# Kernel optimization log

Hardware: AMD Instinct MI355X
Metric: run time of the kernel (lower is better)

The kernel has to match this reference:

```python
import jax, jax.numpy as jnp
import numpy as np

HEADS = 16
DIM_HEAD = 64
SCALE = DIM_HEAD ** -0.5


def setup_inputs() -> dict:
    key = jax.random.key(0)
    k1, k2, k3 = jax.random.split(key, 3)
    dim = 1024
    inner = HEADS * DIM_HEAD  # 1024
    x = jax.random.normal(k1, (4, 2048, dim), dtype=jnp.float32)
    # Dense kernels stored as [in, out] like keras; scaled for sane magnitudes
    w_qkv = jax.random.normal(k2, (dim, inner * 3), dtype=jnp.float32) * (dim ** -0.5)
    w_out = jax.random.normal(k3, (inner, dim), dtype=jnp.float32) * (inner ** -0.5)
    b_out = jnp.zeros((dim,), dtype=jnp.float32)
    return {"x": x, "w_qkv": w_qkv, "w_out": w_out, "b_out": b_out}


def reference(x, w_qkv, w_out, b_out):
    b, n, _ = x.shape
    qkv = x @ w_qkv  # [b, n, 3*inner]
    q, k, v = jnp.split(qkv, 3, axis=-1)
    # 'b n (h d) -> b h n d'
    split_heads = lambda t: t.reshape(b, n, HEADS, DIM_HEAD).transpose(0, 2, 1, 3)
    q, k, v = split_heads(q), split_heads(k), split_heads(v)
    dots = jnp.einsum('bhid,bhjd->bhij', q, k) * SCALE  # [b,h,n,n]
    attn = jax.nn.softmax(dots, axis=-1)
    out = jnp.einsum('bhij,bhjd->bhid', attn, v)  # [b,h,n,d]
    out = out.transpose(0, 2, 1, 3).reshape(b, n, HEADS * DIM_HEAD)  # 'b h n d -> b n (h d)'
    # project_out: Dense(dim) + Dropout(0.0) (no-op)
    return out @ w_out + b_out
```

## Files before the change

kernel.cpp:

```cpp
#include <hip/hip_runtime.h>
#include <hip/hip_bf16.h>
#include <stdint.h>

#define BATCH 4
#define SEQ   2048
#define HEADS 16
#define DHEAD 64
#define DIM   1024
#define NQKV  3072
#define ROWS  (BATCH*SEQ)
#define QSCALE 0.18033688011112042f
#define SMAX 12.0f

typedef __attribute__((ext_vector_type(8)))  short short8;
typedef __attribute__((ext_vector_type(4)))  float f32x4;
typedef __attribute__((ext_vector_type(16))) float f32x16;

#if __has_builtin(__builtin_amdgcn_exp2f)
#define EXP2F(x) __builtin_amdgcn_exp2f(x)
#else
#define EXP2F(x) __expf((x) * 0.6931471805599453f)
#endif

typedef const __attribute__((address_space(1))) uint32_t GU32;
typedef __attribute__((address_space(3))) uint32_t LU32;
#define GLLDS16(g, l) __builtin_amdgcn_global_load_lds((GU32*)(g), (LU32*)(l), 16, 0, 0)

__device__ __forceinline__ ushort f2bf(float f) {
    union { float f; uint32_t u; } x; x.f = f;
    uint32_t r = x.u + 0x7fffu + ((x.u >> 16) & 1u);
    return (ushort)(r >> 16);
}

__global__ __launch_bounds__(256) void cvt_x_kernel(
    const float* __restrict__ in, ushort* __restrict__ out, int n8) {
    int i = blockIdx.x * 256 + threadIdx.x;
    if (i >= n8) return;
    f32x4 a = ((const f32x4*)in)[2*i];
    f32x4 b = ((const f32x4*)in)[2*i+1];
    short8 o;
    o[0]=(short)f2bf(a[0]); o[1]=(short)f2bf(a[1]); o[2]=(short)f2bf(a[2]); o[3]=(short)f2bf(a[3]);
    o[4]=(short)f2bf(b[0]); o[5]=(short)f2bf(b[1]); o[6]=(short)f2bf(b[2]); o[7]=(short)f2bf(b[3]);
    ((short8*)out)[i] = o;
}

__global__ __launch_bounds__(256) void transpose_w_kernel(
    const float* __restrict__ in, ushort* __restrict__ out, int R, int C) {
    __shared__ float tile[32][33];
    int ctiles = C >> 5;
    int bx = blockIdx.x % ctiles, by = blockIdx.x / ctiles;
    int c0 = bx << 5, r0 = by << 5;
    int tx = threadIdx.x & 31, ty = threadIdx.x >> 5;
#pragma unroll
    for (int it = 0; it < 4; ++it)
        tile[ty + 8*it][tx] = in[(size_t)(r0 + ty + 8*it)*C + c0 + tx];
    __syncthreads();
#pragma unroll
    for (int it = 0; it < 4; ++it)
        out[(size_t)(c0 + ty + 8*it)*R + r0 + tx] = f2bf(tile[tx][ty + 8*it]);
}

__global__ __launch_bounds__(256) void gemm1_kernel(
    const ushort* __restrict__ A, const ushort* __restrict__ BT,
    ushort* __restrict__ Qo, ushort* __restrict__ Ko, ushort* __restrict__ Vt) {
    const int K = DIM;
    __shared__ ushort As[128][32];
    __shared__ ushort Bs[128][32];
    int t = threadIdx.x;
    int lane = t & 63, wid = t >> 6;
    int lo = lane & 15, hi = lane >> 4;
    int wm = wid >> 1, wn = wid & 1;
    int bx = blockIdx.x % (NQKV/128), by = blockIdx.x / (NQKV/128);
    int m0 = by * 128, n0 = bx * 128;
    int sr = t >> 2, sc = (t & 3) * 8;

    const ushort* ga = A  + (size_t)(m0 + sr) * K + sc;
    const ushort* gb = BT + (size_t)(n0 + sr) * K + sc;
    char* asb = (char*)&As[0][0] + wid * 1024;
    char* bsb = (char*)&Bs[0][0] + wid * 1024;

    f32x4 acc[4][4];
#pragma unroll
    for (int i = 0; i < 4; ++i)
#pragma unroll
        for (int j = 0; j < 4; ++j) acc[i][j] = (f32x4){0.f,0.f,0.f,0.f};

    for (int k0 = 0; k0 < K; k0 += 32) {
        __syncthreads();
        GLLDS16(ga + k0,                asb);
        GLLDS16(ga + (size_t)64*K + k0, asb + 4096);
        GLLDS16(gb + k0,                bsb);
        GLLDS16(gb + (size_t)64*K + k0, bsb + 4096);
        __syncthreads();
        short8 af[4], bf[4];
#pragma unroll
        for (int i = 0; i < 4; ++i) af[i] = *(const short8*)&As[wm*64 + i*16 + lo][hi*8];
#pragma unroll
        for (int j = 0; j < 4; ++j) bf[j] = *(const short8*)&Bs[wn*64 + j*16 + lo][hi*8];
#pragma unroll
        for (int i = 0; i < 4; ++i)
#pragma unroll
            for (int j = 0; j < 4; ++j)
                acc[i][j] = __builtin_amdgcn_mfma_f32_16x16x32_bf16(af[i], bf[j], acc[i][j], 0, 0, 0);
    }

#pragma unroll
    for (int i = 0; i < 4; ++i) {
#pragma unroll
        for (int j = 0; j < 4; ++j) {
            int col = n0 + wn*64 + j*16 + lo;
            int which = col >> 10, cc = col & 1023;
            int h_ = cc >> 6, d_ = cc & 63;
            int rb = m0 + wm*64 + i*16 + hi*4;
            int b_ = rb >> 11, n_ = rb & 2047;
            if (which == 2) {
                uint2 w;
                w.x = (uint32_t)f2bf(acc[i][j][0]) | ((uint32_t)f2bf(acc[i][j][1]) << 16);
                w.y = (uint32_t)f2bf(acc[i][j][2]) | ((uint32_t)f2bf(acc[i][j][3]) << 16);
                *(uint2*)&Vt[(((size_t)(b_*HEADS + h_))*DHEAD + d_)*SEQ + n_] = w;
            } else {
                ushort* dst = (which == 0) ? Qo : Ko;
                float scl = (which == 0) ? QSCALE : 1.0f;
#pragma unroll
                for (int r = 0; r < 4; ++r)
                    dst[(((size_t)(b_*HEADS + h_))*SEQ + n_ + r)*DHEAD + d_] = f2bf(acc[i][j][r] * scl);
            }
        }
    }
}

__global__ __launch_bounds__(256, 2) void attn_kernel(
    const ushort* __restrict__ Q, const ushort* __restrict__ K,
    const ushort* __restrict__ VT, ushort* __restrict__ O) {
    __shared__ ushort Ks[2][8192];

    int t = threadIdx.x;
    int lane = t & 63, wid = t >> 6;
    int l31 = lane & 31, l5 = lane >> 5;
    int bid = blockIdx.x;
    int bh = bid & 63, qb = bid >> 6;
    int q0 = qb * 256 + wid * 64;

    const ushort* QbA = Q  + (size_t)bh * SEQ * DHEAD + (size_t)(q0 + l31) * DHEAD + l5*8;
    const ushort* QbB = QbA + (size_t)32 * DHEAD;
    const ushort* Kbh = K  + (size_t)bh * SEQ * DHEAD;
    const ushort* V0  = VT + (size_t)bh * DHEAD * SEQ + (size_t)l31 * SEQ + l5*8;
    const ushort* V1  = V0 + (size_t)32 * SEQ;

    int rr = t >> 3, c8 = t & 7;
    short8 kreg[4];
#define GLOADK(TT) do { _Pragma("unroll") \
    for (int i = 0; i < 4; ++i) \
        kreg[i] = *(const short8*)(Kbh + ((size_t)((TT)*128 + i*32 + rr))*64 + c8*8); \
} while(0)
#define SWRITEK(BUF) do { _Pragma("unroll") \
    for (int i = 0; i < 4; ++i) \
        *(short8*)((char*)&Ks[BUF][0] + (i*32 + rr)*128 + ((c8*16) ^ ((rr&7)<<4))) = kreg[i]; \
} while(0)

    short8 qfA[4], qfB[4];
#pragma unroll
    for (int ds = 0; ds < 4; ++ds) {
        qfA[ds] = *(const short8*)(QbA + ds*16);
        qfB[ds] = *(const short8*)(QbB + ds*16);
    }

    f32x16 oaA0, oaA1, oaB0, oaB1;
#pragma unroll
    for (int r = 0; r < 16; ++r) { oaA0[r]=0.f; oaA1[r]=0.f; oaB0[r]=0.f; oaB1[r]=0.f; }
    float lA = 0.f, lB = 0.f;

    auto softmax_repack = [&](f32x16& st, float& l_, short8& P1o, short8& P2o) {
        float p[16];
#pragma unroll
        for (int r = 0; r < 16; ++r) p[r] = EXP2F(st[r] - SMAX);
        float s0 = (p[0]+p[1]) + (p[2]+p[3]);
        float s1 = (p[4]+p[5]) + (p[6]+p[7]);
        float s2 = (p[8]+p[9]) + (p[10]+p[11]);
        float s3 = (p[12]+p[13]) + (p[14]+p[15]);
        l_ += (s0+s1) + (s2+s3);
        uint32_t a0,a1,b0,b1,c0,c1,d0,d1;
        asm("v_cvt_pk_bf16_f32 %0, %1, %2" : "=v"(a0) : "v"(p[0]),  "v"(p[1]));
        asm("v_cvt_pk_bf16_f32 %0, %1, %2" : "=v"(a1) : "v"(p[2]),  "v"(p[3]));
        asm("v_cvt_pk_bf16_f32 %0, %1, %2" : "=v"(b0) : "v"(p[4]),  "v"(p[5]));
        asm("v_cvt_pk_bf16_f32 %0, %1, %2" : "=v"(b1) : "v"(p[6]),  "v"(p[7]));
        asm("v_cvt_pk_bf16_f32 %0, %1, %2" : "=v"(c0) : "v"(p[8]),  "v"(p[9]));
        asm("v_cvt_pk_bf16_f32 %0, %1, %2" : "=v"(c1) : "v"(p[10]), "v"(p[11]));
        asm("v_cvt_pk_bf16_f32 %0, %1, %2" : "=v"(d0) : "v"(p[12]), "v"(p[13]));
        asm("v_cvt_pk_bf16_f32 %0, %1, %2" : "=v"(d1) : "v"(p[14]), "v"(p[15]));
        uint32_t s0w = l5 ? a0 : b0, s1w = l5 ? a1 : b1;
        uint32_t r0w = (uint32_t)__shfl_xor((int)s0w, 32, 64);
        uint32_t r1w = (uint32_t)__shfl_xor((int)s1w, 32, 64);
        uint32_t s2w = l5 ? c0 : d0, s3w = l5 ? c1 : d1;
        uint32_t r2w = (uint32_t)__shfl_xor((int)s2w, 32, 64);
        uint32_t r3w = (uint32_t)__shfl_xor((int)s3w, 32, 64);
        union PU { uint32_t u[4]; short8 s8; };
        PU P1, P2;
        P1.u[0] = l5 ? r0w : a0;  P1.u[1] = l5 ? r1w : a1;
        P1.u[2] = l5 ? b0 : r0w;  P1.u[3] = l5 ? b1 : r1w;
        P2.u[0] = l5 ? r2w : c0;  P2.u[1] = l5 ? r3w : c1;
        P2.u[2] = l5 ? d0 : r2w;  P2.u[3] = l5 ? d1 : r3w;
        P1o = P1.s8; P2o = P2.s8;
    };

    GLOADK(0); SWRITEK(0);
    int cur = 0;
    for (int tt = 0; tt < SEQ/128; ++tt) {
        __syncthreads();
        if (tt+1 < SEQ/128) GLOADK(tt+1);
        const char* kb_ = (const char*)&Ks[cur][0];
#pragma unroll 1
        for (int s = 0; s < 4; ++s) {
            int no = tt*128 + s*32;
            short8 vf0 = *(const short8*)(V0 + no);
            short8 vf1 = *(const short8*)(V0 + no + 16);
            short8 vf2_ = *(const short8*)(V1 + no);
            short8 vf3 = *(const short8*)(V1 + no + 16);
            short8 kf[4];
#pragma unroll
            for (int ds = 0; ds < 4; ++ds)
                kf[ds] = *(const short8*)(kb_ + (s*32 + l31)*128
                                          + ((((ds*2 + l5)*16) ^ ((l31&7)<<4))));
            f32x16 stA, stB;
#pragma unroll
            for (int r = 0; r < 16; ++r) { stA[r] = 0.f; stB[r] = 0.f; }
            __builtin_amdgcn_s_setprio(1);
#pragma unroll
            for (int ds = 0; ds < 4; ++ds) {
                stA = __builtin_amdgcn_mfma_f32_32x32x16_bf16(kf[ds], qfA[ds], stA, 0, 0, 0);
                stB = __builtin_amdgcn_mfma_f32_32x32x16_bf16(kf[ds], qfB[ds], stB, 0, 0, 0);
            }
            __builtin_amdgcn_s_setprio(0);
            short8 P1A, P2A, P1B, P2B;
            softmax_repack(stA, lA, P1A, P2A);
            softmax_repack(stB, lB, P1B, P2B);
            __builtin_amdgcn_s_setprio(1);
            oaA0 = __builtin_amdgcn_mfma_f32_32x32x16_bf16(vf0,  P1A, oaA0, 0, 0, 0);
            oaB0 = __builtin_amdgcn_mfma_f32_32x32x16_bf16(vf0,  P1B, oaB0, 0, 0, 0);
            oaA0 = __builtin_amdgcn_mfma_f32_32x32x16_bf16(vf1,  P2A, oaA0, 0, 0, 0);
            oaB0 = __builtin_amdgcn_mfma_f32_32x32x16_bf16(vf1,  P2B, oaB0, 0, 0, 0);
            oaA1 = __builtin_amdgcn_mfma_f32_32x32x16_bf16(vf2_, P1A, oaA1, 0, 0, 0);
            oaB1 = __builtin_amdgcn_mfma_f32_32x32x16_bf16(vf2_, P1B, oaB1, 0, 0, 0);
            oaA1 = __builtin_amdgcn_mfma_f32_32x32x16_bf16(vf3,  P2A, oaA1, 0, 0, 0);
            oaB1 = __builtin_amdgcn_mfma_f32_32x32x16_bf16(vf3,  P2B, oaB1, 0, 0, 0);
            __builtin_amdgcn_s_setprio(0);
            __builtin_amdgcn_sched_barrier(0);
        }
        if (tt+1 < SEQ/128) SWRITEK(cur^1);
        cur ^= 1;
    }

    lA += __shfl_xor(lA, 32, 64);
    lB += __shfl_xor(lB, 32, 64);

    int b_ = bh >> 4, h_ = bh & 15;
    {
        float inv = 1.0f / lA;
        int n_ = q0 + l31;
        ushort* dst = O + ((size_t)(b_*SEQ + n_))*DIM + h_*DHEAD + l5*4;
#pragma unroll
        for (int g = 0; g < 4; ++g) {
            uint2 w;
            w.x = (uint32_t)f2bf(oaA0[4*g]*inv)   | ((uint32_t)f2bf(oaA0[4*g+1]*inv) << 16);
            w.y = (uint32_t)f2bf(oaA0[4*g+2]*inv) | ((uint32_t)f2bf(oaA0[4*g+3]*inv) << 16);
            *(uint2*)(dst + 8*g) = w;
            uint2 w2;
            w2.x = (uint32_t)f2bf(oaA1[4*g]*inv)   | ((uint32_t)f2bf(oaA1[4*g+1]*inv) << 16);
            w2.y = (uint32_t)f2bf(oaA1[4*g+2]*inv) | ((uint32_t)f2bf(oaA1[4*g+3]*inv) << 16);
            *(uint2*)(dst + 32 + 8*g) = w2;
        }
    }
    {
        float inv = 1.0f / lB;
        int n_ = q0 + 32 + l31;
        ushort* dst = O + ((size_t)(b_*SEQ + n_))*DIM + h_*DHEAD + l5*4;
#pragma unroll
        for (int g = 0; g < 4; ++g) {
            uint2 w;
            w.x = (uint32_t)f2bf(oaB0[4*g]*inv)   | ((uint32_t)f2bf(oaB0[4*g+1]*inv) << 16);
            w.y = (uint32_t)f2bf(oaB0[4*g+2]*inv) | ((uint32_t)f2bf(oaB0[4*g+3]*inv) << 16);
            *(uint2*)(dst + 8*g) = w;
            uint2 w2;
            w2.x = (uint32_t)f2bf(oaB1[4*g]*inv)   | ((uint32_t)f2bf(oaB1[4*g+1]*inv) << 16);
            w2.y = (uint32_t)f2bf(oaB1[4*g+2]*inv) | ((uint32_t)f2bf(oaB1[4*g+3]*inv) << 16);
            *(uint2*)(dst + 32 + 8*g) = w2;
        }
    }
}

__global__ __launch_bounds__(256) void gemm2_kernel(
    const ushort* __restrict__ A, const ushort* __restrict__ BT,
    const float* __restrict__ bias, float* __restrict__ Cout) {
    const int K = DIM;
    __shared__ ushort As[128][32];
    __shared__ ushort Bs[128][32];
    int t = threadIdx.x;
    int lane = t & 63, wid = t >> 6;
    int lo = lane & 15, hi = lane >> 4;
    int wm = wid >> 1, wn = wid & 1;
    int bx = blockIdx.x % (DIM/128), by = blockIdx.x / (DIM/128);
    int m0 = by * 128, n0 = bx * 128;
    int sr = t >> 2, sc = (t & 3) * 8;

    const ushort* ga = A  + (size_t)(m0 + sr) * K + sc;
    const ushort* gb = BT + (size_t)(n0 + sr) * K + sc;
    char* asb = (char*)&As[0][0] + wid * 1024;
    char* bsb = (char*)&Bs[0][0] + wid * 1024;

    f32x4 acc[4][4];
#pragma unroll
    for (int i = 0; i < 4; ++i)
#pragma unroll
        for (int j = 0; j < 4; ++j) acc[i][j] = (f32x4){0.f,0.f,0.f,0.f};

    for (int k0 = 0; k0 < K; k0 += 32) {
        __syncthreads();
        GLLDS16(ga + k0,                asb);
        GLLDS16(ga + (size_t)64*K + k0, asb + 4096);
        GLLDS16(gb + k0,                bsb);
        GLLDS16(gb + (size_t)64*K + k0, bsb + 4096);
        __syncthreads();
        short8 af[4], bf[4];
#pragma unroll
        for (int i = 0; i < 4; ++i) af[i] = *(const short8*)&As[wm*64 + i*16 + lo][hi*8];
#pragma unroll
        for (int j = 0; j < 4; ++j) bf[j] = *(const short8*)&Bs[wn*64 + j*16 + lo][hi*8];
#pragma unroll
        for (int i = 0; i < 4; ++i)
#pragma unroll
            for (int j = 0; j < 4; ++j)
                acc[i][j] = __builtin_amdgcn_mfma_f32_16x16x32_bf16(af[i], bf[j], acc[i][j], 0, 0, 0);
    }

#pragma unroll
    for (int i = 0; i < 4; ++i)
#pragma unroll
        for (int j = 0; j < 4; ++j) {
            int col = n0 + wn*64 + j*16 + lo;
            float bv = bias[col];
#pragma unroll
            for (int r = 0; r < 4; ++r) {
                int row = m0 + wm*64 + i*16 + hi*4 + r;
                Cout[(size_t)row*DIM + col] = acc[i][j][r] + bv;
            }
        }
}

extern "C" void kernel_launch(void* const* d_in, const int* in_sizes, int n_in,
                              void* d_out, int out_size, void* d_ws, size_t ws_size,
                              hipStream_t stream) {
    const float* x     = (const float*)d_in[0];
    const float* w_qkv = (const float*)d_in[1];
    const float* w_out = (const float*)d_in[2];
    const float* b_out = (const float*)d_in[3];
    float* out = (float*)d_out;

    char* ws = (char*)d_ws;
    ushort* xb    = (ushort*)(ws);
    ushort* wqkvT = (ushort*)(ws + ((size_t)16 << 20));
    ushort* woutT = (ushort*)(ws + ((size_t)22 << 20));
    ushort* q     = (ushort*)(ws + ((size_t)24 << 20));
    ushort* k     = (ushort*)(ws + ((size_t)40 << 20));
    ushort* vt    = (ushort*)(ws + ((size_t)56 << 20));
    ushort* ao    = (ushort*)(ws + ((size_t)72 << 20));

    cvt_x_kernel<<<(ROWS*DIM/8)/256, 256, 0, stream>>>(x, xb, ROWS*DIM/8);
    transpose_w_kernel<<<(NQKV/32)*(DIM/32), 256, 0, stream>>>(w_qkv, wqkvT, DIM, NQKV);
    transpose_w_kernel<<<(DIM/32)*(DIM/32), 256, 0, stream>>>(w_out, woutT, DIM, DIM);
    gemm1_kernel<<<(NQKV/128)*(ROWS/128), 256, 0, stream>>>(xb, wqkvT, q, k, vt);
    attn_kernel<<<(BATCH*HEADS)*(SEQ/256), 256, 0, stream>>>(q, k, vt, ao);
    gemm2_kernel<<<(DIM/128)*(ROWS/128), 256, 0, stream>>>(ao, woutT, b_out, out);
}
```

Measured before the change: 205.4 us.

## Remove P repack shuffles by permuting V loads; swizzle GEMM blocks per XCD

In attention, the V fragment loads are changed to two 4-element half loads at lane-dependent offsets, so the MFMA k-ordering matches the native layout of the softmax output. This removes the cross-lane shuffles and selects used to repack P, and also drops a sched_barrier. Both GEMMs remap block indices so that consecutive blocks on the same XCD (bid&7) cover contiguous tiles, aiming for better L2 reuse. The cost is twice as many, narrower global V loads.

```diff
diff --git a/kernel.cpp b/kernel.cpp
--- a/kernel.cpp
+++ b/kernel.cpp
@@ -13,6 +13,7 @@
 #define SMAX 12.0f
 
 typedef __attribute__((ext_vector_type(8)))  short short8;
+typedef __attribute__((ext_vector_type(4)))  short short4v;
 typedef __attribute__((ext_vector_type(4)))  float f32x4;
 typedef __attribute__((ext_vector_type(16))) float f32x16;
 
@@ -70,7 +71,9 @@
     int lane = t & 63, wid = t >> 6;
     int lo = lane & 15, hi = lane >> 4;
     int wm = wid >> 1, wn = wid & 1;
-    int bx = blockIdx.x % (NQKV/128), by = blockIdx.x / (NQKV/128);
+    int bid = blockIdx.x;
+    int sw = (bid & 7) * ((NQKV/128)*(ROWS/128)/8) + (bid >> 3);
+    int bx = sw % (NQKV/128), by = sw / (NQKV/128);
     int m0 = by * 128, n0 = bx * 128;
     int sr = t >> 2, sc = (t & 3) * 8;
 
@@ -144,7 +147,7 @@
     const ushort* QbA = Q  + (size_t)bh * SEQ * DHEAD + (size_t)(q0 + l31) * DHEAD + l5*8;
     const ushort* QbB = QbA + (size_t)32 * DHEAD;
     const ushort* Kbh = K  + (size_t)bh * SEQ * DHEAD;
-    const ushort* V0  = VT + (size_t)bh * DHEAD * SEQ + (size_t)l31 * SEQ + l5*8;
+    const ushort* V0  = VT + (size_t)bh * DHEAD * SEQ + (size_t)l31 * SEQ;
     const ushort* V1  = V0 + (size_t)32 * SEQ;
 
     int rr = t >> 3, c8 = t & 7;
@@ -179,27 +182,16 @@
         float s2 = (p[8]+p[9]) + (p[10]+p[11]);
         float s3 = (p[12]+p[13]) + (p[14]+p[15]);
         l_ += (s0+s1) + (s2+s3);
-        uint32_t a0,a1,b0,b1,c0,c1,d0,d1;
-        asm("v_cvt_pk_bf16_f32 %0, %1, %2" : "=v"(a0) : "v"(p[0]),  "v"(p[1]));
-        asm("v_cvt_pk_bf16_f32 %0, %1, %2" : "=v"(a1) : "v"(p[2]),  "v"(p[3]));
-        asm("v_cvt_pk_bf16_f32 %0, %1, %2" : "=v"(b0) : "v"(p[4]),  "v"(p[5]));
-        asm("v_cvt_pk_bf16_f32 %0, %1, %2" : "=v"(b1) : "v"(p[6]),  "v"(p[7]));
-        asm("v_cvt_pk_bf16_f32 %0, %1, %2" : "=v"(c0) : "v"(p[8]),  "v"(p[9]));
-        asm("v_cvt_pk_bf16_f32 %0, %1, %2" : "=v"(c1) : "v"(p[10]), "v"(p[11]));
-        asm("v_cvt_pk_bf16_f32 %0, %1, %2" : "=v"(d0) : "v"(p[12]), "v"(p[13]));
-        asm("v_cvt_pk_bf16_f32 %0, %1, %2" : "=v"(d1) : "v"(p[14]), "v"(p[15]));
-        uint32_t s0w = l5 ? a0 : b0, s1w = l5 ? a1 : b1;
-        uint32_t r0w = (uint32_t)__shfl_xor((int)s0w, 32, 64);
-        uint32_t r1w = (uint32_t)__shfl_xor((int)s1w, 32, 64);
-        uint32_t s2w = l5 ? c0 : d0, s3w = l5 ? c1 : d1;
-        uint32_t r2w = (uint32_t)__shfl_xor((int)s2w, 32, 64);
-        uint32_t r3w = (uint32_t)__shfl_xor((int)s3w, 32, 64);
         union PU { uint32_t u[4]; short8 s8; };
         PU P1, P2;
-        P1.u[0] = l5 ? r0w : a0;  P1.u[1] = l5 ? r1w : a1;
-        P1.u[2] = l5 ? b0 : r0w;  P1.u[3] = l5 ? b1 : r1w;
-        P2.u[0] = l5 ? r2w : c0;  P2.u[1] = l5 ? r3w : c1;
-        P2.u[2] = l5 ? d0 : r2w;  P2.u[3] = l5 ? d1 : r3w;
+        asm("v_cvt_pk_bf16_f32 %0, %1, %2" : "=v"(P1.u[0]) : "v"(p[0]),  "v"(p[1]));
+        asm("v_cvt_pk_bf16_f32 %0, %1, %2" : "=v"(P1.u[1]) : "v"(p[2]),  "v"(p[3]));
+        asm("v_cvt_pk_bf16_f32 %0, %1, %2" : "=v"(P1.u[2]) : "v"(p[4]),  "v"(p[5]));
+        asm("v_cvt_pk_bf16_f32 %0, %1, %2" : "=v"(P1.u[3]) : "v"(p[6]),  "v"(p[7]));
+        asm("v_cvt_pk_bf16_f32 %0, %1, %2" : "=v"(P2.u[0]) : "v"(p[8]),  "v"(p[9]));
+        asm("v_cvt_pk_bf16_f32 %0, %1, %2" : "=v"(P2.u[1]) : "v"(p[10]), "v"(p[11]));
+        asm("v_cvt_pk_bf16_f32 %0, %1, %2" : "=v"(P2.u[2]) : "v"(p[12]), "v"(p[13]));
+        asm("v_cvt_pk_bf16_f32 %0, %1, %2" : "=v"(P2.u[3]) : "v"(p[14]), "v"(p[15]));
         P1o = P1.s8; P2o = P2.s8;
     };
 
@@ -211,11 +203,13 @@
         const char* kb_ = (const char*)&Ks[cur][0];
 #pragma unroll 1
         for (int s = 0; s < 4; ++s) {
-            int no = tt*128 + s*32;
-            short8 vf0 = *(const short8*)(V0 + no);
-            short8 vf1 = *(const short8*)(V0 + no + 16);
-            short8 vf2_ = *(const short8*)(V1 + no);
-            short8 vf3 = *(const short8*)(V1 + no + 16);
+            int no = tt*128 + s*32 + l5*4;
+            union V8 { short4v h[2]; short8 s8; };
+            V8 vf0, vf1, vf2, vf3;
+            vf0.h[0] = *(const short4v*)(V0 + no);      vf0.h[1] = *(const short4v*)(V0 + no + 8);
+            vf1.h[0] = *(const short4v*)(V0 + no + 16); vf1.h[1] = *(const short4v*)(V0 + no + 24);
+            vf2.h[0] = *(const short4v*)(V1 + no);      vf2.h[1] = *(const short4v*)(V1 + no + 8);
+            vf3.h[0] = *(const short4v*)(V1 + no + 16); vf3.h[1] = *(const short4v*)(V1 + no + 24);
             short8 kf[4];
 #pragma unroll
             for (int ds = 0; ds < 4; ++ds)
@@ -235,16 +229,15 @@
             softmax_repack(stA, lA, P1A, P2A);
             softmax_repack(stB, lB, P1B, P2B);
             __builtin_amdgcn_s_setprio(1);
-            oaA0 = __builtin_amdgcn_mfma_f32_32x32x16_bf16(vf0,  P1A, oaA0, 0, 0, 0);
-            oaB0 = __builtin_amdgcn_mfma_f32_32x32x16_bf16(vf0,  P1B, oaB0, 0, 0, 0);
-            oaA0 = __builtin_amdgcn_mfma_f32_32x32x16_bf16(vf1,  P2A, oaA0, 0, 0, 0);
-            oaB0 = __builtin_amdgcn_mfma_f32_32x32x16_bf16(vf1,  P2B, oaB0, 0, 0, 0);
-            oaA1 = __builtin_amdgcn_mfma_f32_32x32x16_bf16(vf2_, P1A, oaA1, 0, 0, 0);
-            oaB1 = __builtin_amdgcn_mfma_f32_32x32x16_bf16(vf2_, P1B, oaB1, 0, 0, 0);
-            oaA1 = __builtin_amdgcn_mfma_f32_32x32x16_bf16(vf3,  P2A, oaA1, 0, 0, 0);
-            oaB1 = __builtin_amdgcn_mfma_f32_32x32x16_bf16(vf3,  P2B, oaB1, 0, 0, 0);
+            oaA0 = __builtin_amdgcn_mfma_f32_32x32x16_bf16(vf0.s8, P1A, oaA0, 0, 0, 0);
+            oaB0 = __builtin_amdgcn_mfma_f32_32x32x16_bf16(vf0.s8, P1B, oaB0, 0, 0, 0);
+            oaA0 = __builtin_amdgcn_mfma_f32_32x32x16_bf16(vf1.s8, P2A, oaA0, 0, 0, 0);
+            oaB0 = __builtin_amdgcn_mfma_f32_32x32x16_bf16(vf1.s8, P2B, oaB0, 0, 0, 0);
+            oaA1 = __builtin_amdgcn_mfma_f32_32x32x16_bf16(vf2.s8, P1A, oaA1, 0, 0, 0);
+            oaB1 = __builtin_amdgcn_mfma_f32_32x32x16_bf16(vf2.s8, P1B, oaB1, 0, 0, 0);
+            oaA1 = __builtin_amdgcn_mfma_f32_32x32x16_bf16(vf3.s8, P2A, oaA1, 0, 0, 0);
+            oaB1 = __builtin_amdgcn_mfma_f32_32x32x16_bf16(vf3.s8, P2B, oaB1, 0, 0, 0);
             __builtin_amdgcn_s_setprio(0);
-            __builtin_amdgcn_sched_barrier(0);
         }
         if (tt+1 < SEQ/128) SWRITEK(cur^1);
         cur ^= 1;
@@ -298,7 +291,9 @@
     int lane = t & 63, wid = t >> 6;
     int lo = lane & 15, hi = lane >> 4;
     int wm = wid >> 1, wn = wid & 1;
-    int bx = blockIdx.x % (DIM/128), by = blockIdx.x / (DIM/128);
+    int bid = blockIdx.x;
+    int sw = (bid & 7) * ((DIM/128)*(ROWS/128)/8) + (bid >> 3);
+    int bx = sw % (DIM/128), by = sw / (DIM/128);
     int m0 = by * 128, n0 = bx * 128;
     int sr = t >> 2, sc = (t & 3) * 8;
 
```

New measurement: 242.9 us. 1.18x slower.
